# Optimization experiments

Hardware: AMD Instinct MI355X
Metric: run time of the kernel (lower is better)

## Reference

```python
import jax, jax.numpy as jnp
import numpy as np


def setup_inputs() -> dict:
    key = jax.random.key(0)
    k1, k2, k3, k4 = jax.random.split(key, 4)
    B, S, IN, OUT, ORG = 8, 4096, 1536, 3072, 4
    fan_in_std = (1.0 / IN) ** 0.5
    x = jax.random.normal(k1, (B, S, IN), dtype=jnp.float32)
    weight = jax.random.normal(k2, (ORG, IN, OUT), dtype=jnp.float32) * fan_in_std
    bias = jax.random.normal(k3, (ORG, OUT), dtype=jnp.float32) * 0.01
    organism_index = jax.random.randint(k4, (B,), 0, ORG, dtype=jnp.int64)
    return {"x": x, "organism_index": organism_index, "weight": weight, "bias": bias}


def reference(x, organism_index, weight, bias):
    # Gather per-sample weight [B, IN, OUT] and bias [B, OUT]
    w = weight[organism_index].astype(x.dtype)          # [B, IN, OUT]
    b = bias[organism_index].astype(x.dtype)            # [B, OUT]
    # x: [B, S, IN] -> [B, S, OUT]; bias broadcast over inner dims
    out = jnp.einsum('bsi,bij->bsj', x, w) + b[:, None, :]
    return out
```

## Files before the change

kernel.cpp:

```cpp
#include <hip/hip_runtime.h>
#include <hip/hip_bf16.h>
#include <stdint.h>

typedef __attribute__((ext_vector_type(4))) float f32x4;
typedef __attribute__((ext_vector_type(8))) short short8;

#define DIM_S 4096
#define DIM_IN 1536
#define DIM_OUT 3072
#define NB 8
#define NORG 4

#define XB_ELEMS (NB * DIM_S * DIM_IN)
#define WT_ELEMS (NORG * DIM_OUT * DIM_IN)
#define WS_NEED ((size_t)(XB_ELEMS + WT_ELEMS) * 2)

__device__ __forceinline__ unsigned short f2bf(float f) {
    union { __hip_bfloat16 h; unsigned short u; } c;
    c.h = __float2bfloat16(f);
    return c.u;
}

__device__ __forceinline__ void gload16(const void* g, void* l) {
    __builtin_amdgcn_global_load_lds(
        (const __attribute__((address_space(1))) unsigned int*)g,
        (__attribute__((address_space(3))) unsigned int*)l, 16, 0, 0);
}

__global__ __launch_bounds__(256) void cvt_x(const float* __restrict__ x,
                                             unsigned short* __restrict__ xb) {
    const int nchunk = XB_ELEMS / 8;
    for (int c = blockIdx.x * 256 + threadIdx.x; c < nchunk; c += gridDim.x * 256) {
        const float4 v0 = *reinterpret_cast<const float4*>(x + (size_t)c * 8);
        const float4 v1 = *reinterpret_cast<const float4*>(x + (size_t)c * 8 + 4);
        union { unsigned short u[8]; short8 v; } p;
        p.u[0] = f2bf(v0.x); p.u[1] = f2bf(v0.y); p.u[2] = f2bf(v0.z); p.u[3] = f2bf(v0.w);
        p.u[4] = f2bf(v1.x); p.u[5] = f2bf(v1.y); p.u[6] = f2bf(v1.z); p.u[7] = f2bf(v1.w);
        *reinterpret_cast<short8*>(xb + (size_t)c * 8) = p.v;
    }
}

__global__ __launch_bounds__(256) void cvt_wt(const float* __restrict__ w,
                                              unsigned short* __restrict__ wt) {
    __shared__ unsigned short T[64][68];
    const int bid = blockIdx.x;
    const int org = bid / (24 * 48);
    const int rem = bid % (24 * 48);
    const int k0 = (rem / 48) * 64;
    const int n0 = (rem % 48) * 64;
    const float* __restrict__ wp = w + (size_t)org * DIM_IN * DIM_OUT;
    unsigned short* __restrict__ op = wt + (size_t)org * DIM_OUT * DIM_IN;
    const int t = threadIdx.x;
    #pragma unroll
    for (int i = 0; i < 4; ++i) {
        const int c = t + 256 * i;
        const int kk = c >> 4, nq = (c & 15) * 4;
        const float4 v = *reinterpret_cast<const float4*>(
            wp + (size_t)(k0 + kk) * DIM_OUT + n0 + nq);
        ushort4 pv;
        pv.x = f2bf(v.x); pv.y = f2bf(v.y); pv.z = f2bf(v.z); pv.w = f2bf(v.w);
        *reinterpret_cast<ushort4*>(&T[kk][nq]) = pv;
    }
    __syncthreads();
    #pragma unroll
    for (int i = 0; i < 2; ++i) {
        const int c = t + 256 * i;
        const int n = c >> 3, k8 = (c & 7) * 8;
        union { unsigned short u[8]; short8 v; } p;
        #pragma unroll
        for (int j = 0; j < 8; ++j) p.u[j] = T[k8 + j][n];
        *reinterpret_cast<short8*>(op + (size_t)(n0 + n) * DIM_IN + k0 + k8) = p.v;
    }
}

__global__ __launch_bounds__(512, 2) void mol_gemm_8p(
    const unsigned short* __restrict__ xb, const int* __restrict__ orgidx,
    const unsigned short* __restrict__ wt, const float* __restrict__ bias,
    float* __restrict__ out)
{
    __shared__ __align__(16) unsigned short LDS[2][4][8192];

    const int tid  = threadIdx.x;
    const int lane = tid & 63;
    const int wave = tid >> 6;
    const int wr = wave >> 2;
    const int wc = wave & 3;
    const int l15 = lane & 15;
    const int q16 = lane >> 4;

    const int bid = blockIdx.x;
    const int id  = (bid & 7) * 192 + (bid >> 3);
    const int row0 = (id / 12) * 256;
    const int col0 = (id % 12) * 256;
    const int batch = row0 >> 12;
    const int org   = orgidx[batch];

    const unsigned short* __restrict__ Abase = xb + (size_t)row0 * DIM_IN;
    const unsigned short* __restrict__ Bbase =
        wt + (size_t)org * DIM_OUT * DIM_IN + (size_t)col0 * DIM_IN;

    const int rA = tid >> 2;
    const int qs = ((tid & 3) ^ (rA & 3) ^ ((rA >> 2) & 1)) * 8;
    const unsigned short* pA0 = Abase + (size_t)rA * DIM_IN + qs;
    const unsigned short* pA1 = Abase + (size_t)(128 + rA) * DIM_IN + qs;
    const unsigned short* pB0 = Bbase + (size_t)rA * DIM_IN + qs;
    const unsigned short* pB1 = Bbase + (size_t)(128 + rA) * DIM_IN + qs;

    const int d0 = wave * 512;
    const int d1 = 4096 + wave * 512;

    const int sw = (l15 & 3) ^ ((l15 >> 2) & 1);
    const int offA0 = ((wr * 128 + l15) * 32 + ((q16 ^ sw) << 3)) * 2;
    const int offB0 = ((wc * 64  + l15) * 32 + ((q16 ^ sw) << 3)) * 2;

    f32x4 acc[8][4] = {};
    short8 af[8], b0, b1;

#define STG(buf, slot, p0, p1, kofs) do {                      \
        gload16((p0) + (kofs), &LDS[buf][slot][d0]);           \
        gload16((p1) + (kofs), &LDS[buf][slot][d1]);           \
    } while (0)

#define RD_A(buf, kk) do {                                                  \
        const char* bA_ = (const char*)(&LDS[buf][kk][0]) + offA0;          \
        _Pragma("unroll")                                                   \
        for (int mi_ = 0; mi_ < 8; ++mi_)                                   \
            af[mi_] = *reinterpret_cast<const short8*>(bA_ + 1024 * mi_);   \
    } while (0)

#define RD_B(buf, kk, h) do {                                               \
        const char* bB_ = (const char*)(&LDS[buf][2 + (kk)][0]) + offB0;    \
        b0 = *reinterpret_cast<const short8*>(bB_ + 1024 * (2 * (h)));      \
        b1 = *reinterpret_cast<const short8*>(bB_ + 1024 * (2 * (h) + 1));  \
    } while (0)

#define MM(h) do {                                                          \
        __builtin_amdgcn_s_setprio(1);                                      \
        _Pragma("unroll")                                                   \
        for (int mi_ = 0; mi_ < 8; ++mi_) {                                 \
            acc[mi_][2*(h)]   = __builtin_amdgcn_mfma_f32_16x16x32_bf16(    \
                af[mi_], b0, acc[mi_][2*(h)], 0, 0, 0);                     \
            acc[mi_][2*(h)+1] = __builtin_amdgcn_mfma_f32_16x16x32_bf16(    \
                af[mi_], b1, acc[mi_][2*(h)+1], 0, 0, 0);                   \
        }                                                                   \
        __builtin_amdgcn_s_setprio(0);                                      \
    } while (0)

#define BAR do { __builtin_amdgcn_s_barrier();                              \
                 asm volatile("" ::: "memory"); } while (0)
#define WAIT8 asm volatile("s_waitcnt vmcnt(8)" ::: "memory")

    STG(0, 0, pA0, pA1, 0);
    STG(0, 2, pB0, pB1, 0);
    STG(0, 1, pA0, pA1, 32);
    STG(0, 3, pB0, pB1, 32);
    STG(1, 0, pA0, pA1, 64);
    STG(1, 2, pB0, pB1, 64);
    WAIT8;
    BAR;

    int kA = 96, kB = 96;

#define TILE(buf, obuf) do {                                                   \
        RD_A(buf, 0); RD_B(buf, 0, 0);                                         \
        STG(obuf, 1, pA0, pA1, kA); if (kA < 1504) kA += 32;                   \
        MM(0); BAR;                                                            \
        RD_B(buf, 0, 1);                                                       \
        STG(obuf, 3, pB0, pB1, kB); if (kB < 1504) kB += 32;                   \
        MM(1); WAIT8; BAR;                                                     \
        RD_A(buf, 1); RD_B(buf, 1, 0);                                         \
        STG(buf, 0, pA0, pA1, kA); if (kA < 1504) kA += 32;                    \
        MM(0); BAR;                                                            \
        RD_B(buf, 1, 1);                                                       \
        STG(buf, 2, pB0, pB1, kB); if (kB < 1504) kB += 32;                    \
        MM(1); WAIT8; BAR;                                                     \
    } while (0)

    #pragma unroll 1
    for (int i = 0; i < 12; ++i) {
        TILE(0, 1);
        TILE(1, 0);
    }

    const float* __restrict__ bptr = bias + (size_t)org * DIM_OUT;
    const int crow = q16 * 4;
    const int ccol = l15;
    #pragma unroll
    for (int ni = 0; ni < 4; ++ni) {
        const int gc = col0 + wc * 64 + ni * 16 + ccol;
        const float bv = bptr[gc];
        #pragma unroll
        for (int mi = 0; mi < 8; ++mi) {
            const int gr = row0 + wr * 128 + mi * 16 + crow;
            #pragma unroll
            for (int r = 0; r < 4; ++r)
                out[(size_t)(gr + r) * DIM_OUT + gc] = acc[mi][ni][r] + bv;
        }
    }
#undef STG
#undef RD_A
#undef RD_B
#undef MM
#undef BAR
#undef WAIT8
#undef TILE
}

#define BM 128
#define BN 128
#define BK 32
#define LDK 40
union BF8 { unsigned short u[8]; short8 v; };

__global__ __launch_bounds__(256) void mol_gemm_fb(
    const float* __restrict__ x, const int* __restrict__ orgidx,
    const float* __restrict__ weight, const float* __restrict__ bias,
    float* __restrict__ out)
{
    __shared__ __align__(16) unsigned short Alds[2][BM][LDK];
    __shared__ __align__(16) unsigned short Blds[2][BN][LDK];

    const int tid  = threadIdx.x;
    const int lane = tid & 63;
    const int wave = tid >> 6;
    const int wr = wave >> 1, wc = wave & 1;

    const int bid = blockIdx.x;
    const int id  = (bid & 7) * 768 + (bid >> 3);
    const int row0 = (id / 24) * BM;
    const int col0 = (id % 24) * BN;

    const int batch = row0 / DIM_S;
    const int org   = orgidx[batch];
    const float* __restrict__ W = weight + (size_t)org * DIM_IN * DIM_OUT;

    f32x4 acc[4][4] = {};
    const int ar  = tid >> 2;
    const int ak8 = (tid & 3) * 8;
    const int bn  = tid & 127;
    const int bg0 = tid >> 7;
    const float* __restrict__ xbase = x + (size_t)row0 * DIM_IN;
    const float* __restrict__ wbase = W + col0 + bn;

    auto stage = [&](int buf, int k0) {
        #pragma unroll
        for (int i = 0; i < 2; ++i) {
            const int r = ar + 64 * i;
            const float* xp = xbase + (size_t)r * DIM_IN + k0 + ak8;
            const float4 v0 = *reinterpret_cast<const float4*>(xp);
            const float4 v1 = *reinterpret_cast<const float4*>(xp + 4);
            BF8 p;
            p.u[0] = f2bf(v0.x); p.u[1] = f2bf(v0.y);
            p.u[2] = f2bf(v0.z); p.u[3] = f2bf(v0.w);
            p.u[4] = f2bf(v1.x); p.u[5] = f2bf(v1.y);
            p.u[6] = f2bf(v1.z); p.u[7] = f2bf(v1.w);
            *reinterpret_cast<short8*>(&Alds[buf][r][ak8]) = p.v;
        }
        #pragma unroll
        for (int j = 0; j < 2; ++j) {
            const int g = bg0 + 2 * j;
            const float* wp = wbase + (size_t)(k0 + 8 * g) * DIM_OUT;
            BF8 p;
            #pragma unroll
            for (int r = 0; r < 8; ++r) p.u[r] = f2bf(wp[(size_t)r * DIM_OUT]);
            *reinterpret_cast<short8*>(&Blds[buf][bn][8 * g]) = p.v;
        }
    };

    stage(0, 0);
    const int nk = DIM_IN / BK;
    const int kq = (lane >> 4) * 8;
    const int lr = lane & 15;

    for (int t = 0; t < nk; ++t) {
        __syncthreads();
        const int cur = t & 1;
        if (t + 1 < nk) stage(cur ^ 1, (t + 1) * BK);
        short8 a[4], b[4];
        #pragma unroll
        for (int mi = 0; mi < 4; ++mi)
            a[mi] = *reinterpret_cast<const short8*>(&Alds[cur][wr * 64 + mi * 16 + lr][kq]);
        #pragma unroll
        for (int ni = 0; ni < 4; ++ni)
            b[ni] = *reinterpret_cast<const short8*>(&Blds[cur][wc * 64 + ni * 16 + lr][kq]);
        #pragma unroll
        for (int mi = 0; mi < 4; ++mi)
            #pragma unroll
            for (int ni = 0; ni < 4; ++ni)
                acc[mi][ni] = __builtin_amdgcn_mfma_f32_16x16x32_bf16(
                    a[mi], b[ni], acc[mi][ni], 0, 0, 0);
    }

    const float* __restrict__ bptr = bias + (size_t)org * DIM_OUT;
    const int crow = (lane >> 4) * 4;
    const int ccol = lane & 15;
    #pragma unroll
    for (int ni = 0; ni < 4; ++ni) {
        const int gc = col0 + wc * 64 + ni * 16 + ccol;
        const float bv = bptr[gc];
        #pragma unroll
        for (int mi = 0; mi < 4; ++mi) {
            const int gr = row0 + wr * 64 + mi * 16 + crow;
            #pragma unroll
            for (int r = 0; r < 4; ++r)
                out[(size_t)(gr + r) * DIM_OUT + gc] = acc[mi][ni][r] + bv;
        }
    }
}

extern "C" void kernel_launch(void* const* d_in, const int* in_sizes, int n_in,
                              void* d_out, int out_size, void* d_ws, size_t ws_size,
                              hipStream_t stream)
{
    const float* x      = (const float*)d_in[0];
    const int*   orgidx = (const int*)d_in[1];
    const float* weight = (const float*)d_in[2];
    const float* bias   = (const float*)d_in[3];
    float* out = (float*)d_out;

    if (ws_size >= WS_NEED) {
        unsigned short* xbp = (unsigned short*)d_ws;
        unsigned short* wtp = xbp + XB_ELEMS;
        cvt_x<<<dim3(2048), dim3(256), 0, stream>>>(x, xbp);
        cvt_wt<<<dim3(NORG * 24 * 48), dim3(256), 0, stream>>>(weight, wtp);
        mol_gemm_8p<<<dim3(1536), dim3(512), 0, stream>>>(xbp, orgidx, wtp, bias, out);
    } else {
        mol_gemm_fb<<<dim3(6144), dim3(256), 0, stream>>>(x, orgidx, weight, bias, out);
    }
}
```

Before: 435.1 us.

## Split MFMA phases by A-row halves and fence LDS reads before compute

Restructures each K-subtile's inner loop so that each phase loads 4 A fragments (half the M rows) and all 4 B fragments, then issues a 4x4 block of MFMAs. Previously each phase read all 8 A fragments and 2 B fragments. It adds a barrier plus sched_barrier between the LDS reads/global stage and the MFMA cluster, giving two barriers per phase. The aim is to cut register pressure and get a cleaner, ping-pong-style separation of memory and compute across waves. The risk is the extra barrier per phase, which may add stalls.

```diff
diff --git a/kernel.cpp b/kernel.cpp
--- a/kernel.cpp
+++ b/kernel.cpp
@@ -114,40 +114,44 @@
     const int offB0 = ((wc * 64  + l15) * 32 + ((q16 ^ sw) << 3)) * 2;
 
     f32x4 acc[8][4] = {};
-    short8 af[8], b0, b1;
+    short8 af4[4], bfr[4];
 
 #define STG(buf, slot, p0, p1, kofs) do {                      \
         gload16((p0) + (kofs), &LDS[buf][slot][d0]);           \
         gload16((p1) + (kofs), &LDS[buf][slot][d1]);           \
     } while (0)
 
-#define RD_A(buf, kk) do {                                                  \
-        const char* bA_ = (const char*)(&LDS[buf][kk][0]) + offA0;          \
+#define RD_A4(buf, kk, mih) do {                                            \
+        const char* bA_ = (const char*)(&LDS[buf][kk][0]) + offA0           \
+                          + 4096 * (mih);                                   \
         _Pragma("unroll")                                                   \
-        for (int mi_ = 0; mi_ < 8; ++mi_)                                   \
-            af[mi_] = *reinterpret_cast<const short8*>(bA_ + 1024 * mi_);   \
-    } while (0)
-
-#define RD_B(buf, kk, h) do {                                               \
+        for (int i_ = 0; i_ < 4; ++i_)                                      \
+            af4[i_] = *reinterpret_cast<const short8*>(bA_ + 1024 * i_);    \
+    } while (0)
+
+#define RD_B4(buf, kk) do {                                                 \
         const char* bB_ = (const char*)(&LDS[buf][2 + (kk)][0]) + offB0;    \
-        b0 = *reinterpret_cast<const short8*>(bB_ + 1024 * (2 * (h)));      \
-        b1 = *reinterpret_cast<const short8*>(bB_ + 1024 * (2 * (h) + 1));  \
-    } while (0)
-
-#define MM(h) do {                                                          \
+        _Pragma("unroll")                                                   \
+        for (int i_ = 0; i_ < 4; ++i_)                                      \
+            bfr[i_] = *reinterpret_cast<const short8*>(bB_ + 1024 * i_);    \
+    } while (0)
+
+#define MM(mih) do {                                                        \
         __builtin_amdgcn_s_setprio(1);                                      \
         _Pragma("unroll")                                                   \
-        for (int mi_ = 0; mi_ < 8; ++mi_) {                                 \
-            acc[mi_][2*(h)]   = __builtin_amdgcn_mfma_f32_16x16x32_bf16(    \
-                af[mi_], b0, acc[mi_][2*(h)], 0, 0, 0);                     \
-            acc[mi_][2*(h)+1] = __builtin_amdgcn_mfma_f32_16x16x32_bf16(    \
-                af[mi_], b1, acc[mi_][2*(h)+1], 0, 0, 0);                   \
+        for (int i_ = 0; i_ < 4; ++i_) {                                    \
+            _Pragma("unroll")                                               \
+            for (int n_ = 0; n_ < 4; ++n_)                                  \
+                acc[(mih)*4 + i_][n_] =                                     \
+                    __builtin_amdgcn_mfma_f32_16x16x32_bf16(                \
+                        af4[i_], bfr[n_], acc[(mih)*4 + i_][n_], 0, 0, 0);  \
         }                                                                   \
         __builtin_amdgcn_s_setprio(0);                                      \
     } while (0)
 
-#define BAR do { __builtin_amdgcn_s_barrier();                              \
-                 asm volatile("" ::: "memory"); } while (0)
+#define BAR  do { __builtin_amdgcn_s_barrier();                             \
+                  asm volatile("" ::: "memory"); } while (0)
+#define SB0  __builtin_amdgcn_sched_barrier(0)
 #define WAIT8 asm volatile("s_waitcnt vmcnt(8)" ::: "memory")
 
     STG(0, 0, pA0, pA1, 0);
@@ -161,19 +165,22 @@
 
     int kA = 96, kB = 96;
 
-#define TILE(buf, obuf) do {                                                   \
-        RD_A(buf, 0); RD_B(buf, 0, 0);                                         \
-        STG(obuf, 1, pA0, pA1, kA); if (kA < 1504) kA += 32;                   \
-        MM(0); BAR;                                                            \
-        RD_B(buf, 0, 1);                                                       \
-        STG(obuf, 3, pB0, pB1, kB); if (kB < 1504) kB += 32;                   \
-        MM(1); WAIT8; BAR;                                                     \
-        RD_A(buf, 1); RD_B(buf, 1, 0);                                         \
-        STG(buf, 0, pA0, pA1, kA); if (kA < 1504) kA += 32;                    \
-        MM(0); BAR;                                                            \
-        RD_B(buf, 1, 1);                                                       \
-        STG(buf, 2, pB0, pB1, kB); if (kB < 1504) kB += 32;                    \
-        MM(1); WAIT8; BAR;                                                     \
+#define PHASE(buf, kk, mih, sbuf, sslot, pp0, pp1, kref, wait8) do {        \
+        RD_A4(buf, kk, mih);                                                \
+        if ((mih) == 0) RD_B4(buf, kk);                                     \
+        STG(sbuf, sslot, pp0, pp1, kref);                                   \
+        if (kref < 1504) kref += 32;                                        \
+        BAR; SB0;                                                           \
+        MM(mih);                                                            \
+        if (wait8) WAIT8;                                                   \
+        BAR;                                                                \
+    } while (0)
+
+#define TILE(buf, obuf) do {                                                \
+        PHASE(buf, 0, 0, obuf, 1, pA0, pA1, kA, 0);                         \
+        PHASE(buf, 0, 1, obuf, 3, pB0, pB1, kB, 1);                         \
+        PHASE(buf, 1, 0, buf,  0, pA0, pA1, kA, 0);                         \
+        PHASE(buf, 1, 1, buf,  2, pB0, pB1, kB, 1);                         \
     } while (0)
 
     #pragma unroll 1
@@ -198,11 +205,13 @@
         }
     }
 #undef STG
-#undef RD_A
-#undef RD_B
+#undef RD_A4
+#undef RD_B4
 #undef MM
 #undef BAR
+#undef SB0
 #undef WAIT8
+#undef PHASE
 #undef TILE
 }
 
```

After: 439.3 us. No clear change (+1.0%).
